# Kernel optimization log

Hardware: AMD Instinct MI355X
Metric: run time of the kernel (lower is better)

The kernel has to match this reference:

```python
import jax, jax.numpy as jnp
import numpy as np

N = 100000   # nodes
E = 800000   # edges
D = 64       # hidden_channels
H = 4        # heads
C = D        # out_channels per head (PyG: out_channels=hidden)


def setup_inputs() -> dict:
    key = jax.random.key(0)
    ks = jax.random.split(key, 20)
    inp = {}
    inp['x'] = jax.random.normal(ks[0], (N, D), dtype=jnp.float32)
    inp['edge_index'] = jax.random.randint(ks[1], (2, E), 0, N, dtype=jnp.int32)
    i = 2
    for layer in (1, 2):
        for nm in ('Wq', 'Wk', 'Wv'):
            inp[f'{nm}{layer}'] = jax.random.normal(ks[i], (D, H * C), dtype=jnp.float32) * 0.05; i += 1
            inp[f'b{nm[1]}{layer}'] = jnp.zeros((H * C,), dtype=jnp.float32)
        inp[f'Ws{layer}'] = jax.random.normal(ks[i], (D, D), dtype=jnp.float32) * 0.05; i += 1
        inp[f'bs{layer}'] = jnp.zeros((D,), dtype=jnp.float32)
    return inp


def _transformer_conv(x, src, dst, Wq, bq, Wk, bk, Wv, bv, Ws, bs):
    n = x.shape[0]
    q = (x @ Wq + bq).reshape(n, H, C)
    k = (x @ Wk + bk).reshape(n, H, C)
    v = (x @ Wv + bv).reshape(n, H, C)
    # per-edge attention logits: [E, H]
    alpha = jnp.einsum('ehc,ehc->eh', q[dst], k[src]) / np.sqrt(C).astype(np.float32)
    # segment softmax over incoming edges of each destination node
    amax = jax.ops.segment_max(alpha, dst, num_segments=n)          # [N, H]
    ex = jnp.exp(alpha - amax[dst])                                 # [E, H]
    denom = jax.ops.segment_sum(ex, dst, num_segments=n)           # [N, H]
    attn = ex / (denom[dst] + 1e-16)                                # [E, H]
    msg = v[src] * attn[:, :, None]                                 # [E, H, C]
    agg = jax.ops.segment_sum(msg, dst, num_segments=n)            # [N, H, C]
    # concat=False -> mean over heads; root_weight skip connection
    return agg.mean(axis=1) + x @ Ws + bs


def reference(x, edge_index, Wq1, bq1, Wk1, bk1, Wv1, bv1, Ws1, bs1,
              Wq2, bq2, Wk2, bk2, Wv2, bv2, Ws2, bs2):
    src, dst = edge_index[0], edge_index[1]
    h = _transformer_conv(x, src, dst, Wq1, bq1, Wk1, bk1, Wv1, bv1, Ws1, bs1)
    h = jax.nn.relu(h)
    out = _transformer_conv(h, src, dst, Wq2, bq2, Wk2, bk2, Wv2, bv2, Ws2, bs2)
    return out
```

## Files before the change

### kernel.cpp

```cpp
#include <hip/hip_runtime.h>
#include <hip/hip_fp16.h>
#include <math.h>


typedef __attribute__((ext_vector_type(8))) short bf16x8;
typedef __attribute__((ext_vector_type(4))) float f32x4;
typedef __attribute__((ext_vector_type(2))) float f32x2;

#define QKSCALE 32.0f
#define C_EXP2 1.760325e-4f

__device__ inline unsigned short f2bf(float f) {
    unsigned int u = __float_as_uint(f);
    u = (u + 0x7fffu + ((u >> 16) & 1u)) >> 16;
    return (unsigned short)u;
}

#if __has_builtin(__builtin_amdgcn_cvt_pk_fp8_f32) && __has_builtin(__builtin_amdgcn_cvt_pk_f32_fp8)
#define HW_FP8 1
#endif

#ifndef HW_FP8
__device__ inline unsigned int fp8_enc1(float f) {
    unsigned int u = __float_as_uint(f);
    unsigned int s = (u >> 24) & 0x80u;
    float a = fabsf(f);
    if (a >= 448.f) return s | 0x7Eu;
    if (a < 0.015625f) return s;
    unsigned int ua = __float_as_uint(a);
    unsigned int r = ua + 0x7FFFFu + ((ua >> 20) & 1u);
    int e = (int)((r >> 23) & 255u) - 120;
    unsigned int m = (r >> 20) & 7u;
    if (e < 1) return s;
    if (e > 15) return s | 0x7Eu;
    return s | (unsigned int)((e << 3) | m);
}
__device__ inline float fp8_dec1(unsigned int b) {
    unsigned int e = (b >> 3) & 15u, m = b & 7u;
    float v;
    if (e) v = __uint_as_float(((e + 120u) << 23) | (m << 20));
    else   v = (float)m * 0.001953125f;
    return (b & 0x80u) ? -v : v;
}
#endif

__device__ inline unsigned int fp8x4_pack(float f0, float f1, float f2, float f3) {
#ifdef HW_FP8
    int pk = __builtin_amdgcn_cvt_pk_fp8_f32(f0, f1, 0, false);
    pk = __builtin_amdgcn_cvt_pk_fp8_f32(f2, f3, pk, true);
    return (unsigned int)pk;
#else
    return fp8_enc1(f0) | (fp8_enc1(f1) << 8) | (fp8_enc1(f2) << 16) | (fp8_enc1(f3) << 24);
#endif
}

__device__ inline float4 fp8x4_unpack(unsigned int k) {
#ifdef HW_FP8
    f32x2 lo = __builtin_amdgcn_cvt_pk_f32_fp8((int)k, false);
    f32x2 hi = __builtin_amdgcn_cvt_pk_f32_fp8((int)k, true);
    return make_float4(lo[0], lo[1], hi[0], hi[1]);
#else
    return make_float4(fp8_dec1(k & 255u), fp8_dec1((k >> 8) & 255u),
                       fp8_dec1((k >> 16) & 255u), fp8_dec1(k >> 24));
#endif
}

__device__ inline unsigned int i8x4_pack(float f0, float f1, float f2, float f3) {
    int a = (int)rintf(f0 * QKSCALE); a = a < -127 ? -127 : (a > 127 ? 127 : a);
    int b = (int)rintf(f1 * QKSCALE); b = b < -127 ? -127 : (b > 127 ? 127 : b);
    int c = (int)rintf(f2 * QKSCALE); c = c < -127 ? -127 : (c > 127 ? 127 : c);
    int d = (int)rintf(f3 * QKSCALE); d = d < -127 ? -127 : (d > 127 ? 127 : d);
    return (unsigned int)((a & 255) | ((b & 255) << 8) | ((c & 255) << 16) | ((d & 255) << 24));
}

__device__ inline int sdot4(unsigned int a, unsigned int b, int c) {
#if __has_builtin(__builtin_amdgcn_sdot4)
    return __builtin_amdgcn_sdot4((int)a, (int)b, c, false);
#else
    int r = c;
#pragma unroll
    for (int i = 0; i < 4; ++i) {
        int ai = (int)(a << (24 - 8 * i)) >> 24;
        int bi = (int)(b << (24 - 8 * i)) >> 24;
        r += ai * bi;
    }
    return r;
#endif
}

__global__ void k_setup(
    const float* __restrict__ x, unsigned short* __restrict__ Xb, int ncast4,
    const float* __restrict__ Wq1, const float* __restrict__ Wk1,
    const float* __restrict__ Wv1, const float* __restrict__ Ws1,
    const float* __restrict__ Wq2, const float* __restrict__ Wk2,
    const float* __restrict__ Wv2, const float* __restrict__ Ws2,
    unsigned short* __restrict__ Wt,
    int* __restrict__ counts, int* __restrict__ cursor, int N, int castBl)
{
    int b = blockIdx.x, tid = threadIdx.x;
    if (b < castBl) {
        int i = b * 256 + tid;
        if (i < ncast4) {
            float4 v = ((const float4*)x)[i];
            ushort4 o;
            o.x = f2bf(v.x); o.y = f2bf(v.y); o.z = f2bf(v.z); o.w = f2bf(v.w);
            ((ushort4*)Xb)[i] = o;
        }
    } else if (b < castBl + 416) {
        int j = (b - castBl) * 256 + tid;
        int layer = j / 53248;
        int r = j % 53248;
        if (r < 49152) {
            int m = r / 16384, w = r % 16384;
            int n = w / 64, k = w % 64;
            const float* W = (layer == 0)
                ? ((m == 0) ? Wq1 : (m == 1) ? Wk1 : Wv1)
                : ((m == 0) ? Wq2 : (m == 1) ? Wk2 : Wv2);
            Wt[layer * 53248 + m * 16384 + n * 64 + k] = f2bf(W[k * 256 + n]);
        } else {
            int w = r - 49152;
            int n = w / 64, k = w % 64;
            const float* W = (layer == 0) ? Ws1 : Ws2;
            Wt[layer * 53248 + 49152 + n * 64 + k] = f2bf(W[k * 64 + n]);
        }
    } else {
        int i = (b - castBl - 416) * 256 + tid;
        if (i < N) { counts[i] = 0; cursor[i] = 0; }
    }
}

__global__ void k_hist(const int* __restrict__ dst, int E, int* __restrict__ counts) {
    int e = blockIdx.x * 256 + threadIdx.x;
    if (e < E) atomicAdd(&counts[dst[e]], 1);
}

#define SCAN_B 256
#define SCAN_CHUNK 2048
__global__ void k_scan1(const int* __restrict__ counts, int n,
                        int* __restrict__ offs, int* __restrict__ bsums) {
    __shared__ int lds[SCAN_B];
    int b = blockIdx.x, tid = threadIdx.x;
    int base = b * SCAN_CHUNK + tid * 8;
    int v[8]; int s = 0;
#pragma unroll
    for (int i = 0; i < 8; ++i) { int idx = base + i; int c = (idx < n) ? counts[idx] : 0; v[i] = s; s += c; }
    lds[tid] = s;
    for (int off = 1; off < SCAN_B; off <<= 1) {
        __syncthreads();
        int x = (tid >= off) ? lds[tid - off] : 0;
        __syncthreads();
        lds[tid] += x;
    }
    __syncthreads();
    int texcl = lds[tid] - s;
#pragma unroll
    for (int i = 0; i < 8; ++i) { int idx = base + i; if (idx < n) offs[idx] = texcl + v[i]; }
    if (tid == SCAN_B - 1) bsums[b] = lds[tid];
}

__global__ void k_scan2(int* bsums, int nb) {
    __shared__ int lds[256];
    int t = threadIdx.x;
    if (nb > 256) {
        if (t == 0) { int s = 0; for (int i = 0; i < nb; ++i) { int c = bsums[i]; bsums[i] = s; s += c; } }
        return;
    }
    int v = (t < nb) ? bsums[t] : 0;
    lds[t] = v;
    for (int off = 1; off < 256; off <<= 1) {
        __syncthreads();
        int x = (t >= off) ? lds[t - off] : 0;
        __syncthreads();
        lds[t] += x;
    }
    __syncthreads();
    if (t < nb) bsums[t] = lds[t] - v;
}

__global__ void k_scatter(const int* __restrict__ src, const int* __restrict__ dst, int E,
                          const int* __restrict__ offs, const int* __restrict__ bsums,
                          int* __restrict__ cursor, int* __restrict__ csr_src) {
    int e = blockIdx.x * 256 + threadIdx.x;
    if (e < E) {
        int d = dst[e];
        int p = offs[d] + bsums[d >> 11] + atomicAdd(&cursor[d], 1);
        csr_src[p] = src[e];
    }
}

#define WSTR 72
__global__ __launch_bounds__(256) void k_mfma_qkvs(
    const unsigned short* __restrict__ Xb, int nrows,
    const unsigned short* __restrict__ WtL,
    const float* __restrict__ bq, const float* __restrict__ bk,
    const float* __restrict__ bv, const float* __restrict__ bs,
    unsigned char* __restrict__ Qb, unsigned char* __restrict__ Kb,
    unsigned char* __restrict__ Vb, unsigned char* __restrict__ Sb)
{
    __shared__ short WtS[256 * WSTR];
    __shared__ short XbS[64 * WSTR];
    int mat = blockIdx.y;
    const unsigned short* Wt = WtL + ((mat < 3) ? mat * 16384 : 49152);
    const float* bias = (mat == 0) ? bq : (mat == 1) ? bk : (mat == 2) ? bv : bs;
    unsigned char* Ob = (mat == 0) ? Qb : (mat == 1) ? Kb : (mat == 2) ? Vb : Sb;
    int tid = threadIdx.x;
    int wave = tid >> 6, lane = tid & 63;
    int quad = lane >> 4, n16 = lane & 15;
    int r0 = blockIdx.x * 64;

    int nrowsW = (mat < 3) ? 256 : 64;
    for (int c = tid; c < nrowsW * 8; c += 256) {
        int row = c >> 3, off = c & 7;
        uint4 v = *(const uint4*)(Wt + row * 64 + off * 8);
        *(uint4*)(&WtS[row * WSTR + off * 8]) = v;
    }
    for (int c = tid; c < 64 * 8; c += 256) {
        int row = c >> 3, off = c & 7;
        int gr = r0 + row; if (gr >= nrows) gr = nrows - 1;
        uint4 v = *(const uint4*)(Xb + (size_t)gr * 64 + off * 8);
        *(uint4*)(&XbS[row * WSTR + off * 8]) = v;
    }
    __syncthreads();

    int ncpw = (mat < 3) ? 4 : 1;
    int ctbase = (mat < 3) ? wave * 4 : wave;
    bf16x8 bf[8];
    float4 bb[4];
#pragma unroll
    for (int c = 0; c < 4; ++c) {
        if (c < ncpw) {
            int ct = ctbase + c;
            const short* wrow = &WtS[(ct * 16 + n16) * WSTR];
            bf[2 * c]     = *(const bf16x8*)(wrow + quad * 8);
            bf[2 * c + 1] = *(const bf16x8*)(wrow + 32 + quad * 8);
            bb[c] = *(const float4*)(bias + ct * 16 + quad * 4);
        }
    }
#pragma unroll
    for (int g = 0; g < 4; ++g) {
        const short* arow = &XbS[(g * 16 + n16) * WSTR];
        bf16x8 a0 = *(const bf16x8*)(arow + quad * 8);
        bf16x8 a1 = *(const bf16x8*)(arow + 32 + quad * 8);
        int node = r0 + g * 16 + n16;
        bool ok = node < nrows;
#pragma unroll
        for (int c = 0; c < 4; ++c) {
            if (c < ncpw) {
                f32x4 acc = {0.f, 0.f, 0.f, 0.f};
                acc = __builtin_amdgcn_mfma_f32_16x16x32_bf16(bf[2 * c], a0, acc, 0, 0, 0);
                acc = __builtin_amdgcn_mfma_f32_16x16x32_bf16(bf[2 * c + 1], a1, acc, 0, 0, 0);
                int ct = ctbase + c;
                int ch0 = ct * 16 + quad * 4;
                float f0 = acc[0] + bb[c].x, f1 = acc[1] + bb[c].y;
                float f2 = acc[2] + bb[c].z, f3 = acc[3] + bb[c].w;
                if (ok) {
                    if (mat < 2) {
                        *(unsigned int*)(Ob + (size_t)node * 256 + ch0) =
                            i8x4_pack(f0, f1, f2, f3);
                    } else if (mat == 2) {
                        *(unsigned int*)(Ob + (size_t)node * 256 + ch0) =
                            fp8x4_pack(f0, f1, f2, f3);
                    } else {
                        *(float4*)(Ob + (size_t)node * 256 + ch0 * 4) =
                            make_float4(f0, f1, f2, f3);
                    }
                }
            }
        }
    }
}

__global__ __launch_bounds__(256) void k_attn(
    const unsigned char* __restrict__ Qb, const unsigned char* __restrict__ Kb,
    const unsigned char* __restrict__ Vb, const unsigned char* __restrict__ Sb,
    const int* __restrict__ offs, const int* __restrict__ bsums,
    const int* __restrict__ csr_src,
    float* __restrict__ out, unsigned short* __restrict__ Xb,
    int n, int Etot, int mode)
{
    int node = blockIdx.x * 4 + (threadIdx.x >> 6);
    if (node >= n) return;
    int lane = threadIdx.x & 63;
    int sl = lane & 31;
    int half = lane >> 5;
    uint2 q8 = *(const uint2*)(Qb + (size_t)node * 256 + sl * 8);
    int beg = offs[node] + bsums[node >> 11];
    int end = (node + 1 < n) ? (offs[node + 1] + bsums[(node + 1) >> 11]) : Etot;
    float l = 0.f;
    float acc[8];
#pragma unroll
    for (int i = 0; i < 8; ++i) acc[i] = 0.f;
    for (int base = beg; base < end; base += 8) {
        int cnt = end - base; if (cnt > 8) cnt = 8;
        int my = (lane < cnt) ? csr_src[base + lane] : 0;
        uint2 kk[4], vv[4];
#pragma unroll
        for (int p = 0; p < 4; ++p) {
            int idx = __shfl(my, 2 * p + half);
            kk[p] = *(const uint2*)(Kb + (size_t)idx * 256 + sl * 8);
            vv[p] = *(const uint2*)(Vb + (size_t)idx * 256 + sl * 8);
        }
#pragma unroll
        for (int p = 0; p < 4; ++p) {
            int d = sdot4(kk[p].x, q8.x, 0);
            d = sdot4(kk[p].y, q8.y, d);
            d += __shfl_xor(d, 1); d += __shfl_xor(d, 2); d += __shfl_xor(d, 4);
            float w = __builtin_exp2f((float)d * C_EXP2);
            w = (2 * p + half < cnt) ? w : 0.f;
            l += w;
            float4 va = fp8x4_unpack(vv[p].x);
            float4 vb = fp8x4_unpack(vv[p].y);
            acc[0] += va.x * w; acc[1] += va.y * w;
            acc[2] += va.z * w; acc[3] += va.w * w;
            acc[4] += vb.x * w; acc[5] += vb.y * w;
            acc[6] += vb.z * w; acc[7] += vb.w * w;
        }
    }
    l += __shfl_xor(l, 32);
#pragma unroll
    for (int i = 0; i < 8; ++i) acc[i] += __shfl_xor(acc[i], 32);
    float inv = 1.f / (l + 1e-16f);
#pragma unroll
    for (int i = 0; i < 8; ++i) acc[i] *= inv;
#pragma unroll
    for (int i = 0; i < 8; ++i) {
        acc[i] += __shfl_xor(acc[i], 8);
        acc[i] += __shfl_xor(acc[i], 16);
        acc[i] *= 0.25f;
    }
    if (lane < 8) {
        float4 s0 = *(const float4*)(Sb + (size_t)node * 256 + lane * 32);
        float4 s1 = *(const float4*)(Sb + (size_t)node * 256 + lane * 32 + 16);
        float r0 = acc[0] + s0.x, r1 = acc[1] + s0.y;
        float r2 = acc[2] + s0.z, r3 = acc[3] + s0.w;
        float r4 = acc[4] + s1.x, r5 = acc[5] + s1.y;
        float r6 = acc[6] + s1.z, r7 = acc[7] + s1.w;
        if (mode == 1) {
            r0 = fmaxf(r0, 0.f); r1 = fmaxf(r1, 0.f);
            r2 = fmaxf(r2, 0.f); r3 = fmaxf(r3, 0.f);
            r4 = fmaxf(r4, 0.f); r5 = fmaxf(r5, 0.f);
            r6 = fmaxf(r6, 0.f); r7 = fmaxf(r7, 0.f);
            uint4 o;
            o.x = (unsigned int)f2bf(r0) | ((unsigned int)f2bf(r1) << 16);
            o.y = (unsigned int)f2bf(r2) | ((unsigned int)f2bf(r3) << 16);
            o.z = (unsigned int)f2bf(r4) | ((unsigned int)f2bf(r5) << 16);
            o.w = (unsigned int)f2bf(r6) | ((unsigned int)f2bf(r7) << 16);
            *(uint4*)(Xb + (size_t)node * 64 + lane * 8) = o;
        } else {
            *(float4*)(out + (size_t)node * 64 + lane * 8) = make_float4(r0, r1, r2, r3);
            *(float4*)(out + (size_t)node * 64 + lane * 8 + 4) = make_float4(r4, r5, r6, r7);
        }
    }
}

extern "C" void kernel_launch(void* const* d_in, const int* in_sizes, int n_in,
                              void* d_out, int out_size, void* d_ws, size_t ws_size,
                              hipStream_t stream)
{
    const float* x  = (const float*)d_in[0];
    const int*   ei = (const int*)d_in[1];
    int N = in_sizes[0] / 64;
    int E = in_sizes[1] / 2;
    const int* srcp = ei;
    const int* dstp = ei + E;
    const float* Wq1 = (const float*)d_in[2],  *bq1 = (const float*)d_in[3];
    const float* Wk1 = (const float*)d_in[4],  *bk1 = (const float*)d_in[5];
    const float* Wv1 = (const float*)d_in[6],  *bv1 = (const float*)d_in[7];
    const float* Ws1 = (const float*)d_in[8],  *bs1 = (const float*)d_in[9];
    const float* Wq2 = (const float*)d_in[10], *bq2 = (const float*)d_in[11];
    const float* Wk2 = (const float*)d_in[12], *bk2 = (const float*)d_in[13];
    const float* Wv2 = (const float*)d_in[14], *bv2 = (const float*)d_in[15];
    const float* Ws2 = (const float*)d_in[16], *bs2 = (const float*)d_in[17];
    float* out = (float*)d_out;

    char* ws = (char*)d_ws;
    size_t off = 0;
    auto alloc = [&](size_t bytes) -> void* {
        void* p = ws + off;
        off = (off + bytes + 255) & ~(size_t)255;
        return p;
    };
    unsigned short* Xb = (unsigned short*)alloc((size_t)N * 64 * 2);
    unsigned char* Qb  = (unsigned char*)alloc(((size_t)N + 64) * 256);
    unsigned char* Kb  = (unsigned char*)alloc(((size_t)N + 64) * 256);
    unsigned char* Vb  = (unsigned char*)alloc(((size_t)N + 64) * 256);
    unsigned char* Sb  = (unsigned char*)alloc(((size_t)N + 64) * 256);
    unsigned short* Wt = (unsigned short*)alloc(2 * 53248 * 2);
    int* counts = (int*)alloc((size_t)N * 4);
    int* cursor = (int*)alloc((size_t)N * 4);
    int* offs   = (int*)alloc((size_t)N * 4);
    int* bsums  = (int*)alloc(1024 * 4);
    int* csr    = (int*)alloc((size_t)E * 4);
    (void)n_in; (void)out_size;
    if (off > ws_size) return;

    int ebl = (E + 255) / 256;
    int nb_scan = (N + SCAN_CHUNK - 1) / SCAN_CHUNK;
    int row_bl = (N + 63) / 64;
    int attn_bl = (N + 3) / 4;
    int ncast4 = N * 16;
    int castBl = (ncast4 + 255) / 256;
    int zeroBl = (N + 255) / 256;

    k_setup<<<castBl + 416 + zeroBl, 256, 0, stream>>>(
        x, Xb, ncast4, Wq1, Wk1, Wv1, Ws1, Wq2, Wk2, Wv2, Ws2, Wt,
        counts, cursor, N, castBl);

    k_hist<<<ebl, 256, 0, stream>>>(dstp, E, counts);
    k_scan1<<<nb_scan, SCAN_B, 0, stream>>>(counts, N, offs, bsums);
    k_scan2<<<1, 256, 0, stream>>>(bsums, nb_scan);
    k_scatter<<<ebl, 256, 0, stream>>>(srcp, dstp, E, offs, bsums, cursor, csr);

    dim3 g4(row_bl, 4);
    k_mfma_qkvs<<<g4, 256, 0, stream>>>(Xb, N, Wt, bq1, bk1, bv1, bs1, Qb, Kb, Vb, Sb);
    k_attn<<<attn_bl, 256, 0, stream>>>(Qb, Kb, Vb, Sb, offs, bsums, csr, out, Xb, N, E, 1);

    k_mfma_qkvs<<<g4, 256, 0, stream>>>(Xb, N, Wt + 53248, bq2, bk2, bv2, bs2, Qb, Kb, Vb, Sb);
    k_attn<<<attn_bl, 256, 0, stream>>>(Qb, Kb, Vb, Sb, offs, bsums, csr, out, Xb, N, E, 0);
}
```

Before: 447.2 us.

## Fuse QKVS GEMMs into one kernel and interleave K/V rows

Merges the four per-matrix GEMM launches (grid y=4) into a single kernel that computes Q, K, V and skip projections per row block. It drops the LDS staging and loads weights and activations straight from global memory into MFMA fragments. K and V are stored interleaved in one 512-byte row per node, so the attention gather reads both from the same row. This removes repeated X loads and LDS traffic and should improve gather locality, but it raises register pressure from holding all weight fragments.

Measured after the change: 461.1 us. +3.1%, slower.

```diff
diff --git a/kernel.cpp b/kernel.cpp
--- a/kernel.cpp
+++ b/kernel.cpp
@@ -188,91 +188,90 @@
     }
 }
 
-#define WSTR 72
-__global__ __launch_bounds__(256) void k_mfma_qkvs(
+__global__ __launch_bounds__(256) void k_gemm(
     const unsigned short* __restrict__ Xb, int nrows,
     const unsigned short* __restrict__ WtL,
-    const float* __restrict__ bq, const float* __restrict__ bk,
-    const float* __restrict__ bv, const float* __restrict__ bs,
-    unsigned char* __restrict__ Qb, unsigned char* __restrict__ Kb,
-    unsigned char* __restrict__ Vb, unsigned char* __restrict__ Sb)
+    const float* __restrict__ bqp, const float* __restrict__ bkp,
+    const float* __restrict__ bvp, const float* __restrict__ bsp,
+    unsigned char* __restrict__ Qb, unsigned char* __restrict__ KVb,
+    unsigned char* __restrict__ Sb)
 {
-    __shared__ short WtS[256 * WSTR];
-    __shared__ short XbS[64 * WSTR];
-    int mat = blockIdx.y;
-    const unsigned short* Wt = WtL + ((mat < 3) ? mat * 16384 : 49152);
-    const float* bias = (mat == 0) ? bq : (mat == 1) ? bk : (mat == 2) ? bv : bs;
-    unsigned char* Ob = (mat == 0) ? Qb : (mat == 1) ? Kb : (mat == 2) ? Vb : Sb;
     int tid = threadIdx.x;
     int wave = tid >> 6, lane = tid & 63;
     int quad = lane >> 4, n16 = lane & 15;
     int r0 = blockIdx.x * 64;
 
-    int nrowsW = (mat < 3) ? 256 : 64;
-    for (int c = tid; c < nrowsW * 8; c += 256) {
-        int row = c >> 3, off = c & 7;
-        uint4 v = *(const uint4*)(Wt + row * 64 + off * 8);
-        *(uint4*)(&WtS[row * WSTR + off * 8]) = v;
-    }
-    for (int c = tid; c < 64 * 8; c += 256) {
-        int row = c >> 3, off = c & 7;
-        int gr = r0 + row; if (gr >= nrows) gr = nrows - 1;
-        uint4 v = *(const uint4*)(Xb + (size_t)gr * 64 + off * 8);
-        *(uint4*)(&XbS[row * WSTR + off * 8]) = v;
-    }
-    __syncthreads();
-
-    int ncpw = (mat < 3) ? 4 : 1;
-    int ctbase = (mat < 3) ? wave * 4 : wave;
-    bf16x8 bf[8];
-    float4 bb[4];
+    const unsigned short* Wq = WtL;
+    const unsigned short* Wk = WtL + 16384;
+    const unsigned short* Wv = WtL + 32768;
+    const unsigned short* Ws = WtL + 49152;
+
+    bf16x8 fQ[8], fK[8], fV[8], fS[2];
+    float4 cQ[4], cK[4], cV[4], cS;
 #pragma unroll
     for (int c = 0; c < 4; ++c) {
-        if (c < ncpw) {
-            int ct = ctbase + c;
-            const short* wrow = &WtS[(ct * 16 + n16) * WSTR];
-            bf[2 * c]     = *(const bf16x8*)(wrow + quad * 8);
-            bf[2 * c + 1] = *(const bf16x8*)(wrow + 32 + quad * 8);
-            bb[c] = *(const float4*)(bias + ct * 16 + quad * 4);
-        }
-    }
+        int ct = wave * 4 + c;
+        int roff = (ct * 16 + n16) * 64 + quad * 8;
+        fQ[2 * c]     = *(const bf16x8*)(Wq + roff);
+        fQ[2 * c + 1] = *(const bf16x8*)(Wq + roff + 32);
+        fK[2 * c]     = *(const bf16x8*)(Wk + roff);
+        fK[2 * c + 1] = *(const bf16x8*)(Wk + roff + 32);
+        fV[2 * c]     = *(const bf16x8*)(Wv + roff);
+        fV[2 * c + 1] = *(const bf16x8*)(Wv + roff + 32);
+        cQ[c] = *(const float4*)(bqp + ct * 16 + quad * 4);
+        cK[c] = *(const float4*)(bkp + ct * 16 + quad * 4);
+        cV[c] = *(const float4*)(bvp + ct * 16 + quad * 4);
+    }
+    {
+        int roff = (wave * 16 + n16) * 64 + quad * 8;
+        fS[0] = *(const bf16x8*)(Ws + roff);
+        fS[1] = *(const bf16x8*)(Ws + roff + 32);
+        cS = *(const float4*)(bsp + wave * 16 + quad * 4);
+    }
+
 #pragma unroll
     for (int g = 0; g < 4; ++g) {
-        const short* arow = &XbS[(g * 16 + n16) * WSTR];
-        bf16x8 a0 = *(const bf16x8*)(arow + quad * 8);
-        bf16x8 a1 = *(const bf16x8*)(arow + 32 + quad * 8);
         int node = r0 + g * 16 + n16;
+        int nodec = (node < nrows) ? node : (nrows - 1);
+        bf16x8 a0 = *(const bf16x8*)(Xb + (size_t)nodec * 64 + quad * 8);
+        bf16x8 a1 = *(const bf16x8*)(Xb + (size_t)nodec * 64 + 32 + quad * 8);
         bool ok = node < nrows;
 #pragma unroll
         for (int c = 0; c < 4; ++c) {
-            if (c < ncpw) {
-                f32x4 acc = {0.f, 0.f, 0.f, 0.f};
-                acc = __builtin_amdgcn_mfma_f32_16x16x32_bf16(bf[2 * c], a0, acc, 0, 0, 0);
-                acc = __builtin_amdgcn_mfma_f32_16x16x32_bf16(bf[2 * c + 1], a1, acc, 0, 0, 0);
-                int ct = ctbase + c;
-                int ch0 = ct * 16 + quad * 4;
-                float f0 = acc[0] + bb[c].x, f1 = acc[1] + bb[c].y;
-                float f2 = acc[2] + bb[c].z, f3 = acc[3] + bb[c].w;
-                if (ok) {
-                    if (mat < 2) {
-                        *(unsigned int*)(Ob + (size_t)node * 256 + ch0) =
-                            i8x4_pack(f0, f1, f2, f3);
-                    } else if (mat == 2) {
-                        *(unsigned int*)(Ob + (size_t)node * 256 + ch0) =
-                            fp8x4_pack(f0, f1, f2, f3);
-                    } else {
-                        *(float4*)(Ob + (size_t)node * 256 + ch0 * 4) =
-                            make_float4(f0, f1, f2, f3);
-                    }
-                }
+            int ch0 = (wave * 4 + c) * 16 + quad * 4;
+            f32x4 aq = {0.f, 0.f, 0.f, 0.f};
+            aq = __builtin_amdgcn_mfma_f32_16x16x32_bf16(fQ[2 * c], a0, aq, 0, 0, 0);
+            aq = __builtin_amdgcn_mfma_f32_16x16x32_bf16(fQ[2 * c + 1], a1, aq, 0, 0, 0);
+            f32x4 ak = {0.f, 0.f, 0.f, 0.f};
+            ak = __builtin_amdgcn_mfma_f32_16x16x32_bf16(fK[2 * c], a0, ak, 0, 0, 0);
+            ak = __builtin_amdgcn_mfma_f32_16x16x32_bf16(fK[2 * c + 1], a1, ak, 0, 0, 0);
+            f32x4 av = {0.f, 0.f, 0.f, 0.f};
+            av = __builtin_amdgcn_mfma_f32_16x16x32_bf16(fV[2 * c], a0, av, 0, 0, 0);
+            av = __builtin_amdgcn_mfma_f32_16x16x32_bf16(fV[2 * c + 1], a1, av, 0, 0, 0);
+            if (ok) {
+                *(unsigned int*)(Qb + (size_t)node * 256 + ch0) =
+                    i8x4_pack(aq[0] + cQ[c].x, aq[1] + cQ[c].y, aq[2] + cQ[c].z, aq[3] + cQ[c].w);
+                *(unsigned int*)(KVb + (size_t)node * 512 + ch0) =
+                    i8x4_pack(ak[0] + cK[c].x, ak[1] + cK[c].y, ak[2] + cK[c].z, ak[3] + cK[c].w);
+                *(unsigned int*)(KVb + (size_t)node * 512 + 256 + ch0) =
+                    fp8x4_pack(av[0] + cV[c].x, av[1] + cV[c].y, av[2] + cV[c].z, av[3] + cV[c].w);
             }
         }
+        {
+            int ch0 = wave * 16 + quad * 4;
+            f32x4 as = {0.f, 0.f, 0.f, 0.f};
+            as = __builtin_amdgcn_mfma_f32_16x16x32_bf16(fS[0], a0, as, 0, 0, 0);
+            as = __builtin_amdgcn_mfma_f32_16x16x32_bf16(fS[1], a1, as, 0, 0, 0);
+            if (ok)
+                *(float4*)(Sb + (size_t)node * 256 + ch0 * 4) =
+                    make_float4(as[0] + cS.x, as[1] + cS.y, as[2] + cS.z, as[3] + cS.w);
+        }
     }
 }
 
 __global__ __launch_bounds__(256) void k_attn(
-    const unsigned char* __restrict__ Qb, const unsigned char* __restrict__ Kb,
-    const unsigned char* __restrict__ Vb, const unsigned char* __restrict__ Sb,
+    const unsigned char* __restrict__ Qb, const unsigned char* __restrict__ KVb,
+    const unsigned char* __restrict__ Sb,
     const int* __restrict__ offs, const int* __restrict__ bsums,
     const int* __restrict__ csr_src,
     float* __restrict__ out, unsigned short* __restrict__ Xb,
@@ -297,8 +296,9 @@
 #pragma unroll
         for (int p = 0; p < 4; ++p) {
             int idx = __shfl(my, 2 * p + half);
-            kk[p] = *(const uint2*)(Kb + (size_t)idx * 256 + sl * 8);
-            vv[p] = *(const uint2*)(Vb + (size_t)idx * 256 + sl * 8);
+            const unsigned char* row = KVb + (size_t)idx * 512 + sl * 8;
+            kk[p] = *(const uint2*)(row);
+            vv[p] = *(const uint2*)(row + 256);
         }
 #pragma unroll
         for (int p = 0; p < 4; ++p) {
@@ -329,8 +329,9 @@
         acc[i] *= 0.25f;
     }
     if (lane < 8) {
-        float4 s0 = *(const float4*)(Sb + (size_t)node * 256 + lane * 32);
-        float4 s1 = *(const float4*)(Sb + (size_t)node * 256 + lane * 32 + 16);
+        const float* Srow = (const float*)(Sb + (size_t)node * 256);
+        float4 s0 = *(const float4*)(Srow + lane * 8);
+        float4 s1 = *(const float4*)(Srow + lane * 8 + 4);
         float r0 = acc[0] + s0.x, r1 = acc[1] + s0.y;
         float r2 = acc[2] + s0.z, r3 = acc[3] + s0.w;
         float r4 = acc[4] + s1.x, r5 = acc[5] + s1.y;
@@ -382,8 +383,7 @@
     };
     unsigned short* Xb = (unsigned short*)alloc((size_t)N * 64 * 2);
     unsigned char* Qb  = (unsigned char*)alloc(((size_t)N + 64) * 256);
-    unsigned char* Kb  = (unsigned char*)alloc(((size_t)N + 64) * 256);
-    unsigned char* Vb  = (unsigned char*)alloc(((size_t)N + 64) * 256);
+    unsigned char* KVb = (unsigned char*)alloc(((size_t)N + 64) * 512);
     unsigned char* Sb  = (unsigned char*)alloc(((size_t)N + 64) * 256);
     unsigned short* Wt = (unsigned short*)alloc(2 * 53248 * 2);
     int* counts = (int*)alloc((size_t)N * 4);
@@ -411,10 +411,9 @@
     k_scan2<<<1, 256, 0, stream>>>(bsums, nb_scan);
     k_scatter<<<ebl, 256, 0, stream>>>(srcp, dstp, E, offs, bsums, cursor, csr);
 
-    dim3 g4(row_bl, 4);
-    k_mfma_qkvs<<<g4, 256, 0, stream>>>(Xb, N, Wt, bq1, bk1, bv1, bs1, Qb, Kb, Vb, Sb);
-    k_attn<<<attn_bl, 256, 0, stream>>>(Qb, Kb, Vb, Sb, offs, bsums, csr, out, Xb, N, E, 1);
-
-    k_mfma_qkvs<<<g4, 256, 0, stream>>>(Xb, N, Wt + 53248, bq2, bk2, bv2, bs2, Qb, Kb, Vb, Sb);
-    k_attn<<<attn_bl, 256, 0, stream>>>(Qb, Kb, Vb, Sb, offs, bsums, csr, out, Xb, N, E, 0);
-}
+    k_gemm<<<row_bl, 256, 0, stream>>>(Xb, N, Wt, bq1, bk1, bv1, bs1, Qb, KVb, Sb);
+    k_attn<<<attn_bl, 256, 0, stream>>>(Qb, KVb, Sb, offs, bsums, csr, out, Xb, N, E, 1);
+
+    k_gemm<<<row_bl, 256, 0, stream>>>(Xb, N, Wt + 53248, bq2, bk2, bv2, bs2, Qb, KVb, Sb);
+    k_attn<<<attn_bl, 256, 0, stream>>>(Qb, KVb, Sb, offs, bsums, csr, out, Xb, N, E, 0);
+}
```
